# Kernel tuning notes

Measured on AMD Instinct MI355X. Metric: run time of the kernel, lower is better.

Reference implementation:

```python
import jax, jax.numpy as jnp
import numpy as np

N_EMBED = 384
HEAD_SIZE = 64


def setup_inputs() -> dict:
    key = jax.random.key(0)
    ks = jax.random.split(key, 7)
    B, T, C = 512, 256, N_EMBED
    inp = jax.random.normal(ks[0], (B, T, C), dtype=jnp.float32)
    s = 1.0 / np.sqrt(C)
    Wv = jax.random.normal(ks[1], (C, HEAD_SIZE), dtype=jnp.float32) * s
    bv = jax.random.normal(ks[2], (HEAD_SIZE,), dtype=jnp.float32) * 0.02
    Wk = jax.random.normal(ks[3], (C, HEAD_SIZE), dtype=jnp.float32) * s
    bk = jax.random.normal(ks[4], (HEAD_SIZE,), dtype=jnp.float32) * 0.02
    Wq = jax.random.normal(ks[5], (C, HEAD_SIZE), dtype=jnp.float32) * s
    bq = jax.random.normal(ks[6], (HEAD_SIZE,), dtype=jnp.float32) * 0.02
    return {"inp": inp, "Wv": Wv, "bv": bv, "Wk": Wk, "bk": bk, "Wq": Wq, "bq": bq}


def reference(inp, Wv, bv, Wk, bk, Wq, bq):
    B, T, C = inp.shape
    values = inp @ Wv + bv   # [B, T, H]
    keys = inp @ Wk + bk     # [B, T, H]
    queries = inp @ Wq + bq  # [B, T, H]
    # Faithful to source: scores = keys @ queries^T, scaled by C**-0.5 (embed dim)
    scale = C ** (-0.5)
    W = jnp.einsum('bth,bsh->bts', keys, queries) * scale  # [B, T, T]
    causal = jnp.tril(jnp.ones((T, T), dtype=bool))
    W = jnp.where(causal, W, -jnp.inf)
    W = jax.nn.softmax(W, axis=-1)
    out = jnp.einsum('bts,bsh->bth', W, values)  # [B, T, H]
    return out
```

## Files before the change

kernel.cpp:

```cpp
#include <hip/hip_runtime.h>
#include <stdint.h>

typedef short s16x8 __attribute__((ext_vector_type(8)));
typedef float f32x4 __attribute__((ext_vector_type(4)));

#define TT 256
#define CC 384
#define HH 64

__device__ __forceinline__ unsigned short f2bf(float f) {
  union { float f; uint32_t u; } v; v.f = f;
  return (unsigned short)((v.u + 0x7fffu + ((v.u >> 16) & 1u)) >> 16);
}

__global__ __launch_bounds__(256, 1) void attn_head_kernel(
    const float* __restrict__ inp,
    const float* __restrict__ Wv, const float* __restrict__ bv,
    const float* __restrict__ Wk, const float* __restrict__ bk,
    const float* __restrict__ Wq, const float* __restrict__ bq,
    float* __restrict__ out)
{
  __shared__ unsigned short inp_lds[256][40];
  __shared__ unsigned short wt_lds[192][40];
  __shared__ unsigned short K_lds[256 * 64];
  __shared__ unsigned short Q_lds[256 * 64];
  __shared__ unsigned short V_lds[64 * 256];
  __shared__ unsigned short P_lds[4][16][40];

  const int b    = blockIdx.x;
  const int tid  = threadIdx.x;
  const int wave = tid >> 6;
  const int lane = tid & 63;
  const int l15  = lane & 15;
  const int lg   = lane >> 4;

  const float* inp_b = inp + (size_t)b * TT * CC;

  f32x4 acc[4][12];
#pragma unroll
  for (int mf = 0; mf < 4; ++mf)
#pragma unroll
    for (int nf = 0; nf < 12; ++nf)
      acc[mf][nf] = (f32x4){0.f, 0.f, 0.f, 0.f};

  for (int k0 = 0; k0 < CC; k0 += 32) {
    __syncthreads();
#pragma unroll
    for (int it = 0; it < 8; ++it) {
      int idx = tid + it * 256;
      int row = idx >> 3, c4 = idx & 7;
      float4 v = *(const float4*)(inp_b + row * CC + k0 + c4 * 4);
      unsigned short* d = &inp_lds[row][c4 * 4];
      d[0] = f2bf(v.x); d[1] = f2bf(v.y); d[2] = f2bf(v.z); d[3] = f2bf(v.w);
    }
#pragma unroll
    for (int m = 0; m < 3; ++m) {
      const float* W = (m == 0) ? Wk : (m == 1 ? Wq : Wv);
#pragma unroll
      for (int it = 0; it < 2; ++it) {
        int idx = tid + it * 256;
        int kk = idx >> 4, c4 = idx & 15;
        float4 v = *(const float4*)(W + (k0 + kk) * HH + c4 * 4);
        int nb = m * 64 + c4 * 4;
        wt_lds[nb + 0][kk] = f2bf(v.x);
        wt_lds[nb + 1][kk] = f2bf(v.y);
        wt_lds[nb + 2][kk] = f2bf(v.z);
        wt_lds[nb + 3][kk] = f2bf(v.w);
      }
    }
    __syncthreads();
    const int t0base = wave * 64;
    s16x8 bb[12];
#pragma unroll
    for (int nf = 0; nf < 12; ++nf)
      bb[nf] = *(const s16x8*)&wt_lds[nf * 16 + l15][lg * 8];
#pragma unroll
    for (int mf = 0; mf < 4; ++mf) {
      s16x8 a = *(const s16x8*)&inp_lds[t0base + mf * 16 + l15][lg * 8];
#pragma unroll
      for (int nf = 0; nf < 12; ++nf)
        acc[mf][nf] = __builtin_amdgcn_mfma_f32_16x16x32_bf16(a, bb[nf], acc[mf][nf], 0, 0, 0);
    }
  }

  {
    const float scale = 0.05103103630798287f;
    const int t0base = wave * 64;
    char* Kb = (char*)K_lds; char* Qb = (char*)Q_lds; char* Vb = (char*)V_lds;
#pragma unroll
    for (int nf = 0; nf < 12; ++nf) {
      int n = nf * 16 + l15;
      float bias = (n < 64) ? bk[n] : (n < 128 ? bq[n - 64] : bv[n - 128]);
#pragma unroll
      for (int mf = 0; mf < 4; ++mf) {
#pragma unroll
        for (int r = 0; r < 4; ++r) {
          int t = t0base + mf * 16 + lg * 4 + r;
          float x = acc[mf][nf][r] + bias;
          if (n < 64) {
            int off = t * 128 + ((n * 2) ^ ((t & 7) << 4));
            *(unsigned short*)(Kb + off) = f2bf(x * scale);
          } else if (n < 128) {
            int nn = n - 64;
            int off = t * 128 + ((nn * 2) ^ ((t & 7) << 4));
            *(unsigned short*)(Qb + off) = f2bf(x);
          } else {
            int nn = n - 128;
            int off = nn * 512 + ((t * 2) ^ ((nn & 7) << 4));
            *(unsigned short*)(Vb + off) = f2bf(x);
          }
        }
      }
    }
  }
  __syncthreads();

  const char* Kb = (const char*)K_lds;
  const char* Qb = (const char*)Q_lds;
  const char* Vb = (const char*)V_lds;

  for (int ti = 0; ti < 4; ++ti) {
    const int tf = ((ti & 1) ? (7 - wave) : wave) + 8 * (ti >> 1);
    const int t0 = tf * 16;
    float m[4], lsum[4];
    f32x4 O[4];
#pragma unroll
    for (int r = 0; r < 4; ++r) { m[r] = -1e30f; lsum[r] = 0.f; }
#pragma unroll
    for (int nf = 0; nf < 4; ++nf) O[nf] = (f32x4){0.f, 0.f, 0.f, 0.f};

    const int trow = t0 + l15;
    const int swzT = (trow & 7) << 4;

    for (int s0 = 0; s0 < t0 + 16; s0 += 32) {
      f32x4 Sa = {0.f,0.f,0.f,0.f}, Sb = {0.f,0.f,0.f,0.f};
      const int srow = s0 + l15;
      const int swzS = (srow & 7) << 4;
#pragma unroll
      for (int kk = 0; kk < 2; ++kk) {
        int hb = (kk * 32 + lg * 8) * 2;
        s16x8 a  = *(const s16x8*)(Kb + trow * 128 + (hb ^ swzT));
        s16x8 q0 = *(const s16x8*)(Qb + srow * 128 + (hb ^ swzS));
        s16x8 q1 = *(const s16x8*)(Qb + (srow + 16) * 128 + (hb ^ swzS));
        Sa = __builtin_amdgcn_mfma_f32_16x16x32_bf16(a, q0, Sa, 0, 0, 0);
        Sb = __builtin_amdgcn_mfma_f32_16x16x32_bf16(a, q1, Sb, 0, 0, 0);
      }
      float alpha[4], pa[4], pb[4];
#pragma unroll
      for (int r = 0; r < 4; ++r) {
        int t = t0 + lg * 4 + r;
        int sA = s0 + l15;
        float xa = (sA      <= t) ? Sa[r] : -1e30f;
        float xb = (sA + 16 <= t) ? Sb[r] : -1e30f;
        float mx = fmaxf(xa, xb);
#pragma unroll
        for (int d = 1; d < 16; d <<= 1) mx = fmaxf(mx, __shfl_xor(mx, d, 64));
        float mn = fmaxf(m[r], mx);
        alpha[r] = __expf(m[r] - mn);
        m[r] = mn;
        pa[r] = __expf(xa - mn);
        pb[r] = __expf(xb - mn);
        float rs = pa[r] + pb[r];
#pragma unroll
        for (int d = 1; d < 16; d <<= 1) rs += __shfl_xor(rs, d, 64);
        lsum[r] = lsum[r] * alpha[r] + rs;
      }
#pragma unroll
      for (int nf = 0; nf < 4; ++nf)
#pragma unroll
        for (int r = 0; r < 4; ++r) O[nf][r] *= alpha[r];
#pragma unroll
      for (int r = 0; r < 4; ++r) {
        int prow = lg * 4 + r;
        P_lds[wave][prow][l15]      = f2bf(pa[r]);
        P_lds[wave][prow][l15 + 16] = f2bf(pb[r]);
      }
      asm volatile("s_waitcnt lgkmcnt(0)" ::: "memory");
      s16x8 pfrag = *(const s16x8*)&P_lds[wave][l15][lg * 8];
#pragma unroll
      for (int nf = 0; nf < 4; ++nf) {
        int h = nf * 16 + l15;
        int sbyte = (s0 + lg * 8) * 2;
        s16x8 vb = *(const s16x8*)(Vb + h * 512 + (sbyte ^ ((h & 7) << 4)));
        O[nf] = __builtin_amdgcn_mfma_f32_16x16x32_bf16(pfrag, vb, O[nf], 0, 0, 0);
      }
    }
    float* outb = out + ((size_t)b * TT + t0) * HH;
#pragma unroll
    for (int r = 0; r < 4; ++r) {
      float inv = 1.0f / lsum[r];
#pragma unroll
      for (int nf = 0; nf < 4; ++nf)
        outb[(lg * 4 + r) * HH + nf * 16 + l15] = O[nf][r] * inv;
    }
  }
}

extern "C" void kernel_launch(void* const* d_in, const int* in_sizes, int n_in,
                              void* d_out, int out_size, void* d_ws, size_t ws_size,
                              hipStream_t stream) {
  (void)n_in; (void)out_size; (void)d_ws; (void)ws_size;
  const float* inp = (const float*)d_in[0];
  const float* Wv  = (const float*)d_in[1];
  const float* bv  = (const float*)d_in[2];
  const float* Wk  = (const float*)d_in[3];
  const float* bk  = (const float*)d_in[4];
  const float* Wq  = (const float*)d_in[5];
  const float* bq  = (const float*)d_in[6];
  float* out = (float*)d_out;
  const int B = in_sizes[0] / (TT * CC);
  attn_head_kernel<<<B, 256, 0, stream>>>(inp, Wv, bv, Wk, bk, Wq, bq, out);
}
```

Baseline: 352.7 us.

## Prepack bf16 weights, use 1024-thread blocks with double-buffered async weight loads

Adds a prepack kernel that transposes the Q/K/V weights to bf16 and folds the scale into Wk and bk. The main kernel grows to 16 waves per block: the projection is split four ways across N, and each wave handles one query tile in the attention phase. The input and weight chunks are double-buffered, with register prefetch for the input and global_load_lds for the weights. This targets low occupancy and serialized load-convert-compute, at the cost of an extra launch and one larger shared LDS buffer.

```diff
diff --git a/kernel.cpp b/kernel.cpp
--- a/kernel.cpp
+++ b/kernel.cpp
@@ -7,25 +7,47 @@
 #define TT 256
 #define CC 384
 #define HH 64
+#define NTOT 192
 
 __device__ __forceinline__ unsigned short f2bf(float f) {
   union { float f; uint32_t u; } v; v.f = f;
   return (unsigned short)((v.u + 0x7fffu + ((v.u >> 16) & 1u)) >> 16);
 }
 
-__global__ __launch_bounds__(256, 1) void attn_head_kernel(
-    const float* __restrict__ inp,
-    const float* __restrict__ Wv, const float* __restrict__ bv,
-    const float* __restrict__ Wk, const float* __restrict__ bk,
-    const float* __restrict__ Wq, const float* __restrict__ bq,
-    float* __restrict__ out)
+__device__ __forceinline__ void gload_lds16(const void* g, void* l) {
+  __builtin_amdgcn_global_load_lds(
+      (const __attribute__((address_space(1))) unsigned int*)g,
+      (__attribute__((address_space(3))) unsigned int*)l, 16, 0, 0);
+}
+
+__global__ void prepack_kernel(const float* __restrict__ Wv, const float* __restrict__ bv,
+                               const float* __restrict__ Wk, const float* __restrict__ bk,
+                               const float* __restrict__ Wq, const float* __restrict__ bq,
+                               unsigned short* __restrict__ WT, float* __restrict__ biases) {
+  const float scale = 0.05103103630798287f;
+  int id = blockIdx.x * 256 + threadIdx.x;
+  if (id < NTOT * CC) {
+    int n = id / CC, k = id % CC;
+    int type = n >> 6, h = n & 63;
+    const float* W = (type == 0) ? Wk : (type == 1 ? Wq : Wv);
+    float v = W[k * HH + h];
+    if (type == 0) v *= scale;
+    WT[id] = f2bf(v);
+  }
+  if (id < NTOT) {
+    int type = id >> 6, h = id & 63;
+    const float* bb = (type == 0) ? bk : (type == 1 ? bq : bv);
+    float v = bb[h];
+    if (type == 0) v *= scale;
+    biases[id] = v;
+  }
+}
+
+__global__ __launch_bounds__(1024, 4) void attn_head_kernel(
+    const float* __restrict__ inp, const unsigned short* __restrict__ WT,
+    const float* __restrict__ biases, float* __restrict__ out)
 {
-  __shared__ unsigned short inp_lds[256][40];
-  __shared__ unsigned short wt_lds[192][40];
-  __shared__ unsigned short K_lds[256 * 64];
-  __shared__ unsigned short Q_lds[256 * 64];
-  __shared__ unsigned short V_lds[64 * 256];
-  __shared__ unsigned short P_lds[4][16][40];
+  __shared__ char lds[118784];
 
   const int b    = blockIdx.x;
   const int tid  = threadIdx.x;
@@ -33,81 +55,94 @@
   const int lane = tid & 63;
   const int l15  = lane & 15;
   const int lg   = lane >> 4;
+  const int tw   = wave >> 2;
+  const int nw   = wave & 3;
 
   const float* inp_b = inp + (size_t)b * TT * CC;
-
-  f32x4 acc[4][12];
+  char* inpbuf0 = lds;          char* inpbuf1 = lds + 16384;
+  char* wtbuf0  = lds + 32768;  char* wtbuf1  = lds + 48128;
+
+  f32x4 acc[4][3];
 #pragma unroll
   for (int mf = 0; mf < 4; ++mf)
 #pragma unroll
-    for (int nf = 0; nf < 12; ++nf)
+    for (int nf = 0; nf < 3; ++nf)
       acc[mf][nf] = (f32x4){0.f, 0.f, 0.f, 0.f};
 
-  for (int k0 = 0; k0 < CC; k0 += 32) {
+  const int srow = tid >> 2;
+  const int sk8  = (tid & 3) * 8;
+  const int sunit = (tid & 3) ^ ((srow >> 1) & 3);
+
+  const int wg = wave * 64 + lane;
+  const int wn = wg / 5;
+  const int wu = wg % 5;
+  const int wuu = (wu == 4) ? 0 : wu;
+  const unsigned short* wsrc_base = WT + wn * CC + wuu * 8;
+
+  float4 r0, r1;
+  r0 = *(const float4*)(inp_b + srow * CC + sk8);
+  r1 = *(const float4*)(inp_b + srow * CC + sk8 + 4);
+  if (wave < 15) gload_lds16(wsrc_base, wtbuf0 + wave * 1024);
+
+  for (int c = 0; c < 12; ++c) {
+    char* ib = (c & 1) ? inpbuf1 : inpbuf0;
+    char* wb = (c & 1) ? wtbuf1 : wtbuf0;
+    asm volatile("s_waitcnt vmcnt(0)" ::: "memory");
+    {
+      union { s16x8 v; unsigned short s[8]; } p;
+      p.s[0] = f2bf(r0.x); p.s[1] = f2bf(r0.y); p.s[2] = f2bf(r0.z); p.s[3] = f2bf(r0.w);
+      p.s[4] = f2bf(r1.x); p.s[5] = f2bf(r1.y); p.s[6] = f2bf(r1.z); p.s[7] = f2bf(r1.w);
+      *(s16x8*)(ib + srow * 64 + sunit * 16) = p.v;
+    }
+    if (c < 11) {
+      int k0 = (c + 1) * 32;
+      r0 = *(const float4*)(inp_b + srow * CC + k0 + sk8);
+      r1 = *(const float4*)(inp_b + srow * CC + k0 + sk8 + 4);
+    }
     __syncthreads();
-#pragma unroll
-    for (int it = 0; it < 8; ++it) {
-      int idx = tid + it * 256;
-      int row = idx >> 3, c4 = idx & 7;
-      float4 v = *(const float4*)(inp_b + row * CC + k0 + c4 * 4);
-      unsigned short* d = &inp_lds[row][c4 * 4];
-      d[0] = f2bf(v.x); d[1] = f2bf(v.y); d[2] = f2bf(v.z); d[3] = f2bf(v.w);
-    }
-#pragma unroll
-    for (int m = 0; m < 3; ++m) {
-      const float* W = (m == 0) ? Wk : (m == 1 ? Wq : Wv);
-#pragma unroll
-      for (int it = 0; it < 2; ++it) {
-        int idx = tid + it * 256;
-        int kk = idx >> 4, c4 = idx & 15;
-        float4 v = *(const float4*)(W + (k0 + kk) * HH + c4 * 4);
-        int nb = m * 64 + c4 * 4;
-        wt_lds[nb + 0][kk] = f2bf(v.x);
-        wt_lds[nb + 1][kk] = f2bf(v.y);
-        wt_lds[nb + 2][kk] = f2bf(v.z);
-        wt_lds[nb + 3][kk] = f2bf(v.w);
-      }
-    }
-    __syncthreads();
-    const int t0base = wave * 64;
-    s16x8 bb[12];
-#pragma unroll
-    for (int nf = 0; nf < 12; ++nf)
-      bb[nf] = *(const s16x8*)&wt_lds[nf * 16 + l15][lg * 8];
+    if (c < 11 && wave < 15)
+      gload_lds16(wsrc_base + (c + 1) * 32, ((c & 1) ? wtbuf0 : wtbuf1) + wave * 1024);
+    s16x8 bb[3];
+#pragma unroll
+    for (int nf = 0; nf < 3; ++nf) {
+      int n = nw * 48 + nf * 16 + l15;
+      bb[nf] = *(const s16x8*)(wb + n * 80 + lg * 16);
+    }
 #pragma unroll
     for (int mf = 0; mf < 4; ++mf) {
-      s16x8 a = *(const s16x8*)&inp_lds[t0base + mf * 16 + l15][lg * 8];
-#pragma unroll
-      for (int nf = 0; nf < 12; ++nf)
+      int t = tw * 64 + mf * 16 + l15;
+      int unit = lg ^ ((t >> 1) & 3);
+      s16x8 a = *(const s16x8*)(ib + t * 64 + unit * 16);
+#pragma unroll
+      for (int nf = 0; nf < 3; ++nf)
         acc[mf][nf] = __builtin_amdgcn_mfma_f32_16x16x32_bf16(a, bb[nf], acc[mf][nf], 0, 0, 0);
     }
   }
 
+  __syncthreads();
+
   {
-    const float scale = 0.05103103630798287f;
-    const int t0base = wave * 64;
-    char* Kb = (char*)K_lds; char* Qb = (char*)Q_lds; char* Vb = (char*)V_lds;
-#pragma unroll
-    for (int nf = 0; nf < 12; ++nf) {
-      int n = nf * 16 + l15;
-      float bias = (n < 64) ? bk[n] : (n < 128 ? bq[n - 64] : bv[n - 128]);
+    char* Kb = lds; char* Qb = lds + 32768; char* Vb = lds + 65536;
+    float bias[3];
+#pragma unroll
+    for (int nf = 0; nf < 3; ++nf) bias[nf] = biases[nw * 48 + nf * 16 + l15];
+#pragma unroll
+    for (int nf = 0; nf < 3; ++nf) {
+      int n = nw * 48 + nf * 16 + l15;
 #pragma unroll
       for (int mf = 0; mf < 4; ++mf) {
 #pragma unroll
         for (int r = 0; r < 4; ++r) {
-          int t = t0base + mf * 16 + lg * 4 + r;
-          float x = acc[mf][nf][r] + bias;
+          int t = tw * 64 + mf * 16 + lg * 4 + r;
+          unsigned short hv = f2bf(acc[mf][nf][r] + bias[nf]);
           if (n < 64) {
-            int off = t * 128 + ((n * 2) ^ ((t & 7) << 4));
-            *(unsigned short*)(Kb + off) = f2bf(x * scale);
+            *(unsigned short*)(Kb + t * 128 + ((n * 2) ^ ((t & 7) << 4))) = hv;
           } else if (n < 128) {
             int nn = n - 64;
-            int off = t * 128 + ((nn * 2) ^ ((t & 7) << 4));
-            *(unsigned short*)(Qb + off) = f2bf(x);
+            *(unsigned short*)(Qb + t * 128 + ((nn * 2) ^ ((t & 7) << 4))) = hv;
           } else {
             int nn = n - 128;
-            int off = nn * 512 + ((t * 2) ^ ((nn & 7) << 4));
-            *(unsigned short*)(Vb + off) = f2bf(x);
+            *(unsigned short*)(Vb + nn * 512 + ((t * 2) ^ ((nn & 7) << 4))) = hv;
           }
         }
       }
@@ -115,12 +150,14 @@
   }
   __syncthreads();
 
-  const char* Kb = (const char*)K_lds;
-  const char* Qb = (const char*)Q_lds;
-  const char* Vb = (const char*)V_lds;
-
-  for (int ti = 0; ti < 4; ++ti) {
-    const int tf = ((ti & 1) ? (7 - wave) : wave) + 8 * (ti >> 1);
+  const char* Kb = lds;
+  const char* Qb = lds + 32768;
+  const char* Vb = lds + 65536;
+  char* Pw = lds + 98304 + wave * 1280;
+
+  {
+    const int gi = wave & 3, ii = wave >> 2;
+    const int tf = (gi < 2) ? (ii * 2 + (ii >> 1) * 8 + gi) : (4 + ii * 2 + (gi - 2));
     const int t0 = tf * 16;
     float m[4], lsum[4];
     f32x4 O[4];
@@ -134,14 +171,14 @@
 
     for (int s0 = 0; s0 < t0 + 16; s0 += 32) {
       f32x4 Sa = {0.f,0.f,0.f,0.f}, Sb = {0.f,0.f,0.f,0.f};
-      const int srow = s0 + l15;
-      const int swzS = (srow & 7) << 4;
+      const int srw = s0 + l15;
+      const int swzS = (srw & 7) << 4;
 #pragma unroll
       for (int kk = 0; kk < 2; ++kk) {
         int hb = (kk * 32 + lg * 8) * 2;
         s16x8 a  = *(const s16x8*)(Kb + trow * 128 + (hb ^ swzT));
-        s16x8 q0 = *(const s16x8*)(Qb + srow * 128 + (hb ^ swzS));
-        s16x8 q1 = *(const s16x8*)(Qb + (srow + 16) * 128 + (hb ^ swzS));
+        s16x8 q0 = *(const s16x8*)(Qb + srw * 128 + (hb ^ swzS));
+        s16x8 q1 = *(const s16x8*)(Qb + (srw + 16) * 128 + (hb ^ swzS));
         Sa = __builtin_amdgcn_mfma_f32_16x16x32_bf16(a, q0, Sa, 0, 0, 0);
         Sb = __builtin_amdgcn_mfma_f32_16x16x32_bf16(a, q1, Sb, 0, 0, 0);
       }
@@ -172,11 +209,12 @@
 #pragma unroll
       for (int r = 0; r < 4; ++r) {
         int prow = lg * 4 + r;
-        P_lds[wave][prow][l15]      = f2bf(pa[r]);
-        P_lds[wave][prow][l15 + 16] = f2bf(pb[r]);
+        *(unsigned short*)(Pw + prow * 80 + l15 * 2)      = f2bf(pa[r]);
+        *(unsigned short*)(Pw + prow * 80 + l15 * 2 + 32) = f2bf(pb[r]);
       }
       asm volatile("s_waitcnt lgkmcnt(0)" ::: "memory");
-      s16x8 pfrag = *(const s16x8*)&P_lds[wave][l15][lg * 8];
+      __builtin_amdgcn_sched_barrier(0);
+      s16x8 pfrag = *(const s16x8*)(Pw + l15 * 80 + lg * 16);
 #pragma unroll
       for (int nf = 0; nf < 4; ++nf) {
         int h = nf * 16 + l15;
@@ -199,7 +237,7 @@
 extern "C" void kernel_launch(void* const* d_in, const int* in_sizes, int n_in,
                               void* d_out, int out_size, void* d_ws, size_t ws_size,
                               hipStream_t stream) {
-  (void)n_in; (void)out_size; (void)d_ws; (void)ws_size;
+  (void)n_in; (void)out_size; (void)ws_size;
   const float* inp = (const float*)d_in[0];
   const float* Wv  = (const float*)d_in[1];
   const float* bv  = (const float*)d_in[2];
@@ -208,6 +246,11 @@
   const float* Wq  = (const float*)d_in[5];
   const float* bq  = (const float*)d_in[6];
   float* out = (float*)d_out;
+
+  unsigned short* WT = (unsigned short*)d_ws;
+  float* biases = (float*)((char*)d_ws + NTOT * CC * 2);
+
   const int B = in_sizes[0] / (TT * CC);
-  attn_head_kernel<<<B, 256, 0, stream>>>(inp, Wv, bv, Wk, bk, Wq, bq, out);
-}
+  prepack_kernel<<<(NTOT * CC + 255) / 256, 256, 0, stream>>>(Wv, bv, Wk, bk, Wq, bq, WT, biases);
+  attn_head_kernel<<<B, 1024, 0, stream>>>(inp, WT, biases, out);
+}
```

After: 331.0 us. 6.1% less time.
